# Kernel tuning notes

Hardware: AMD Instinct MI355X
Metric: run time of the kernel (lower is better)

The kernel has to match this reference:

```python
import jax, jax.numpy as jnp
import numpy as np

# dims
B, N, D = 2, 4096, 384
NUM_HEADS, KEY_DIM, VALUE_DIM = 8, 48, 48
TOP_K = 128
IDX_HEADS, IDX_DIM = 2, 32
SCALE = KEY_DIM ** (-0.5)


def setup_inputs() -> dict:
    key = jax.random.key(0)
    ks = jax.random.split(key, 9)
    def xavier(k, shape):
        fan_in, fan_out = shape[0], shape[1]
        lim = (6.0 / (fan_in + fan_out)) ** 0.5
        return jax.random.uniform(k, shape, jnp.float32, -lim, lim)
    return {
        "x": jax.random.normal(ks[0], (B, N, D), jnp.float32),
        # lightning indexer params
        "wq_idx": xavier(ks[1], (D, IDX_HEADS * IDX_DIM)),
        "wk_idx": xavier(ks[2], (D, IDX_DIM)),
        "ww_idx": xavier(ks[3], (D, IDX_HEADS)),
        # attention params (stored as (in, out) for x @ W)
        "wq": xavier(ks[4], (D, NUM_HEADS * KEY_DIM)),
        "wk": xavier(ks[5], (D, KEY_DIM)),
        "wv": xavier(ks[6], (D, VALUE_DIM)),
        "wo": xavier(ks[7], (NUM_HEADS * VALUE_DIM, D)),
    }


def _forward(x, wq_idx, wk_idx, ww_idx, wq, wk, wv, wo):
    b, n, d = x.shape
    # ---- Lightning indexer: I[q,s] = sum_h w[q,h] * relu(qi[q,h] . ki[s]) ----
    qi = (x @ wq_idx).reshape(b, n, IDX_HEADS, IDX_DIM)      # (B,N,Hi,dki)
    ki = x @ wk_idx                                           # (B,N,dki)
    w_idx = x @ ww_idx                                        # (B,N,Hi)
    raw = jax.nn.relu(jnp.einsum('bqhd,bsd->bqhs', qi, ki))   # (B,Nq,Hi,Nk)
    index_scores = jnp.einsum('bqhs,bqh->bqs', raw, w_idx)    # (B,Nq,Nk)

    # ---- MQA projections ----
    q = (x @ wq).reshape(b, n, NUM_HEADS, KEY_DIM).transpose(0, 2, 1, 3)  # (B,H,N,dk)
    k = x @ wk                                                # (B,N,dk) single KV head
    v = x @ wv                                                # (B,N,dv)

    # ---- top-k select + gather ----
    kk = min(TOP_K, n)
    _, top_idx = jax.lax.top_k(index_scores, kk)              # (B,Nq,k)
    bidx = jnp.arange(b)[:, None, None]
    sel_k = k[bidx, top_idx]                                  # (B,Nq,k,dk)
    sel_v = v[bidx, top_idx]                                  # (B,Nq,k,dv)

    # ---- sparse attention over selected keys ----
    attn = jnp.einsum('bhqd,bqkd->bhqk', q, sel_k) * SCALE    # (B,H,Nq,k)
    probs = jax.nn.softmax(attn, axis=-1)
    out = jnp.einsum('bhqk,bqkd->bhqd', probs, sel_v)         # (B,H,Nq,dv)
    out = out.transpose(0, 2, 1, 3).reshape(b, n, NUM_HEADS * VALUE_DIM)
    return out @ wo                                           # (B,N,D)


def reference(x, wq_idx, wk_idx, ww_idx, wq, wk, wv, wo):
    return _forward(x, wq_idx, wk_idx, ww_idx, wq, wk, wv, wo)
```

## Files before the change

### kernel.cpp

```cpp
#include <hip/hip_runtime.h>
#include <math.h>

#define NB 2
#define NSEQ 4096
#define DMODEL 384
#define NH 8
#define DKQ 48
#define DV 48
#define TOPK 128
#define NQ (NB*NSEQ)

#define QKV_COLS 480
#define C_Q 0
#define C_K 384
#define C_V 432
#define IDX_COLS 128
#define P_QI 0
#define P_KI 64
#define P_W  96
#define ATT_SCALE 0.14433756729740643f

typedef double v4d  __attribute__((ext_vector_type(4)));
typedef float  f32x4 __attribute__((ext_vector_type(4)));
typedef short  s16x8 __attribute__((ext_vector_type(8)));

__device__ inline void bsplit(float v, unsigned short& h, unsigned short& l) {
    unsigned hb = __float_as_uint(v);
    unsigned short hi = (unsigned short)((hb + 0x7FFFu + ((hb >> 16) & 1u)) >> 16);
    float hf = __uint_as_float(((unsigned)hi) << 16);
    float r = v - hf;
    unsigned rb = __float_as_uint(r);
    unsigned short lo = (unsigned short)((rb + 0x7FFFu + ((rb >> 16) & 1u)) >> 16);
    h = hi; l = lo;
}

__global__ void k_split(const float* __restrict__ x,
                        unsigned short* __restrict__ xhi, unsigned short* __restrict__ xlo) {
    int i = blockIdx.x * 256 + threadIdx.x;
    if (i < NQ * DMODEL) {
        unsigned short h, l;
        bsplit(x[i], h, l);
        xhi[i] = h; xlo[i] = l;
    }
}

__global__ void k_concat(const float* __restrict__ wq_idx, const float* __restrict__ wk_idx,
                         const float* __restrict__ ww_idx, const float* __restrict__ wq,
                         const float* __restrict__ wk, const float* __restrict__ wv,
                         const float* __restrict__ wo,
                         unsigned short* __restrict__ WqT_hi, unsigned short* __restrict__ WqT_lo,
                         unsigned short* __restrict__ WoT_hi, unsigned short* __restrict__ WoT_lo,
                         float* __restrict__ Wi_cat) {
    int i = blockIdx.x * 256 + threadIdx.x;
    const int NQK = QKV_COLS * DMODEL;
    const int NWO = DMODEL * DMODEL;
    if (i < NQK) {
        int n = i / DMODEL, k = i % DMODEL;
        float v;
        if (n < 384)      v = wq[(size_t)k*384 + n];
        else if (n < 432) v = wk[(size_t)k*48 + (n-384)];
        else              v = wv[(size_t)k*48 + (n-432)];
        unsigned short h, l; bsplit(v, h, l);
        WqT_hi[i] = h; WqT_lo[i] = l;
    } else if (i < NQK + NWO) {
        int j = i - NQK;
        int n = j / DMODEL, k = j % DMODEL;
        float v = wo[(size_t)k*384 + n];
        unsigned short h, l; bsplit(v, h, l);
        WoT_hi[j] = h; WoT_lo[j] = l;
    } else if (i < NQK + NWO + DMODEL*IDX_COLS) {
        int j = i - NQK - NWO;
        int d = j / IDX_COLS, c = j % IDX_COLS;
        float v;
        if (c < 64)       v = wq_idx[d*64 + c];
        else if (c < 96)  v = wk_idx[d*32 + (c-64)];
        else if (c < 98)  v = ww_idx[d*2 + (c-96)];
        else              v = 0.f;
        Wi_cat[j] = v;
    }
}

#define GLDK 40
__global__ __launch_bounds__(256) void k_gemm_mfma(
        const unsigned short* __restrict__ Ahi, const unsigned short* __restrict__ Alo,
        const unsigned short* __restrict__ Bhi, const unsigned short* __restrict__ Blo,
        float* __restrict__ C, int N, int ldc) {
    __shared__ unsigned short At[2][128][GLDK];
    __shared__ unsigned short Bt[2][64][GLDK];
    const int t = threadIdx.x;
    const int lane = t & 63, wid = t >> 6;
    const int row0 = blockIdx.y * 128, col0 = blockIdx.x * 64;
    const int ml = lane & 15, kq = lane >> 4;
    const int wm = (wid & 1) * 64, wn = (wid >> 1) * 32;

    unsigned short mv = (unsigned short)(__float_as_uint((float)(ml + 1)) >> 16);
    unsigned short one = 0x3F80;
    s16x8 pa, pb;
    #pragma unroll
    for (int j = 0; j < 8; j++) { pa[j] = (short)mv; pb[j] = (short)one; }
    f32x4 zf = (f32x4){0.f, 0.f, 0.f, 0.f};
    f32x4 rowp = __builtin_amdgcn_mfma_f32_16x16x32_bf16(pa, pb, zf, 0, 0, 0);
    f32x4 colp = __builtin_amdgcn_mfma_f32_16x16x32_bf16(pb, pa, zf, 0, 0, 0);
    int rowm[4], colm[4];
    #pragma unroll
    for (int r = 0; r < 4; r++) {
        rowm[r] = (((int)(rowp[r] * 0.03125f + 0.5f)) - 1) & 15;
        colm[r] = (((int)(colp[r] * 0.03125f + 0.5f)) - 1) & 15;
    }

    f32x4 acc[4][2];
    #pragma unroll
    for (int mt = 0; mt < 4; mt++)
        #pragma unroll
        for (int nt = 0; nt < 2; nt++) acc[mt][nt] = zf;

    for (int k0 = 0; k0 < DMODEL; k0 += 32) {
        #pragma unroll
        for (int i = 0; i < 4; i++) {
            int ch = t + 256*i;
            int arr = ch >> 9, rem = ch & 511;
            int r = rem >> 2, p = rem & 3;
            const unsigned short* src = arr ? Alo : Ahi;
            *(int4*)&At[arr][r][p*8] = *(const int4*)(src + (size_t)(row0 + r)*DMODEL + k0 + p*8);
        }
        #pragma unroll
        for (int i = 0; i < 2; i++) {
            int ch = t + 256*i;
            int arr = ch >> 8, rem = ch & 255;
            int r = rem >> 2, p = rem & 3;
            const unsigned short* src = arr ? Blo : Bhi;
            int gc = col0 + r;
            int4 v = {0, 0, 0, 0};
            if (gc < N) v = *(const int4*)(src + (size_t)gc*DMODEL + k0 + p*8);
            *(int4*)&Bt[arr][r][p*8] = v;
        }
        __syncthreads();
        s16x8 af[4][2], bfr[2][2];
        #pragma unroll
        for (int mt = 0; mt < 4; mt++)
            #pragma unroll
            for (int h = 0; h < 2; h++)
                af[mt][h] = *(const s16x8*)&At[h][wm + mt*16 + ml][kq*8];
        #pragma unroll
        for (int nt = 0; nt < 2; nt++)
            #pragma unroll
            for (int h = 0; h < 2; h++)
                bfr[nt][h] = *(const s16x8*)&Bt[h][wn + nt*16 + ml][kq*8];
        #pragma unroll
        for (int mt = 0; mt < 4; mt++)
            #pragma unroll
            for (int nt = 0; nt < 2; nt++) {
                acc[mt][nt] = __builtin_amdgcn_mfma_f32_16x16x32_bf16(af[mt][0], bfr[nt][0], acc[mt][nt], 0, 0, 0);
                acc[mt][nt] = __builtin_amdgcn_mfma_f32_16x16x32_bf16(af[mt][0], bfr[nt][1], acc[mt][nt], 0, 0, 0);
                acc[mt][nt] = __builtin_amdgcn_mfma_f32_16x16x32_bf16(af[mt][1], bfr[nt][0], acc[mt][nt], 0, 0, 0);
            }
        __syncthreads();
    }
    #pragma unroll
    for (int mt = 0; mt < 4; mt++)
        #pragma unroll
        for (int nt = 0; nt < 2; nt++)
            #pragma unroll
            for (int r = 0; r < 4; r++) {
                int rr = row0 + wm + mt*16 + rowm[r];
                int cc = col0 + wn + nt*16 + colm[r];
                if (cc < N) C[(size_t)rr*ldc + cc] = acc[mt][nt][r];
            }
}

__global__ __launch_bounds__(256) void k_proj64(const float* __restrict__ A,
                                                const float* __restrict__ W,
                                                double* __restrict__ P) {
    __shared__ float At[16][32];
    __shared__ float Bt[16][IDX_COLS];
    const int t  = threadIdx.x;
    const int tx = t & 15;
    const int ty = t >> 4;
    const int row0 = blockIdx.x * 32;
    double acc[2][8] = {};

    for (int k0 = 0; k0 < DMODEL; k0 += 16) {
        if (t < 128) {
            int m = t >> 2, kc = t & 3;
            float4 a = *(const float4*)(A + (size_t)(row0 + m)*DMODEL + k0 + kc*4);
            At[kc*4+0][m] = a.x; At[kc*4+1][m] = a.y;
            At[kc*4+2][m] = a.z; At[kc*4+3][m] = a.w;
        }
        for (int i = 0; i < 2; i++) {
            int lin = t + i*256;
            int kk = lin >> 5, c4 = lin & 31;
            float4 b = *(const float4*)(W + (size_t)(k0+kk)*IDX_COLS + c4*4);
            *(float4*)&Bt[kk][c4*4] = b;
        }
        __syncthreads();
        for (int kk = 0; kk < 16; kk++) {
            float a2[2], b8[8];
            a2[0] = At[kk][ty*2]; a2[1] = At[kk][ty*2+1];
            *(float4*)&b8[0] = *(const float4*)&Bt[kk][tx*8];
            *(float4*)&b8[4] = *(const float4*)&Bt[kk][tx*8+4];
            for (int i = 0; i < 2; i++)
                for (int j = 0; j < 8; j++)
                    acc[i][j] += (double)a2[i] * (double)b8[j];
        }
        __syncthreads();
    }
    for (int i = 0; i < 2; i++)
        for (int j = 0; j < 8; j++)
            P[(size_t)(row0 + ty*2 + i)*IDX_COLS + tx*8 + j] = acc[i][j];
}

__global__ __launch_bounds__(256) void k_score_mfma(const double* __restrict__ P,
                                                    unsigned int* __restrict__ K32,
                                                    unsigned int* __restrict__ L32,
                                                    int qstart) {
    __shared__ double A0[32][33];
    __shared__ double A1[32][33];
    __shared__ double Bk[32][129];
    __shared__ double wsh[2][32];
    const int t = threadIdx.x;
    const int lane = t & 63;
    const int wid = t >> 6;
    const int g0 = qstart + blockIdx.y * 32;
    const int b  = g0 / NSEQ;
    const int s0 = blockIdx.x * 128;

    for (int i = 0; i < 8; i++) {
        int lin = t + i*256;
        int q = lin >> 6, c = lin & 63;
        double v = P[(size_t)(g0 + q)*IDX_COLS + P_QI + c];
        if (c < 32) A0[c][q] = v; else A1[c-32][q] = v;
    }
    for (int i = 0; i < 16; i++) {
        int lin = t + i*256;
        int s = lin >> 5, c = lin & 31;
        Bk[c][s] = P[(size_t)(b*NSEQ + s0 + s)*IDX_COLS + P_KI + c];
    }
    if (t < 64) wsh[t & 1][t >> 1] = P[(size_t)(g0 + (t >> 1))*IDX_COLS + P_W + (t & 1)];

    const int qw = (wid & 1) * 16;
    const int sw = (wid >> 1) * 64;
    const int ml = lane & 15;
    const int kl = lane >> 4;

    v4d zero = (v4d){0.0, 0.0, 0.0, 0.0};
    v4d rowp = __builtin_amdgcn_mfma_f64_16x16x4f64((double)(ml+1), 1.0, zero, 0, 0, 0);
    v4d colp = __builtin_amdgcn_mfma_f64_16x16x4f64(1.0, (double)(ml+1), zero, 0, 0, 0);
    int rowm[4], colm[4];
    #pragma unroll
    for (int r = 0; r < 4; r++) {
        rowm[r] = (((int)(rowp[r] * 0.25 + 0.5)) - 1) & 15;
        colm[r] = (((int)(colp[r] * 0.25 + 0.5)) - 1) & 15;
    }

    __syncthreads();

    v4d acc0[4], acc1[4];
    #pragma unroll
    for (int st = 0; st < 4; st++) { acc0[st] = zero; acc1[st] = zero; }

    #pragma unroll
    for (int k4 = 0; k4 < 8; k4++) {
        int k = k4*4 + kl;
        double a0 = A0[k][qw + ml];
        double a1 = A1[k][qw + ml];
        #pragma unroll
        for (int st = 0; st < 4; st++) {
            double bb = Bk[k][sw + st*16 + ml];
            acc0[st] = __builtin_amdgcn_mfma_f64_16x16x4f64(a0, bb, acc0[st], 0, 0, 0);
            acc1[st] = __builtin_amdgcn_mfma_f64_16x16x4f64(a1, bb, acc1[st], 0, 0, 0);
        }
    }

    #pragma unroll
    for (int reg = 0; reg < 4; reg++) {
        int q = qw + rowm[reg];
        double w0 = wsh[0][q], w1 = wsh[1][q];
        #pragma unroll
        for (int st = 0; st < 4; st++) {
            double sc = w0 * fmax(acc0[st][reg], 0.0) + w1 * fmax(acc1[st][reg], 0.0);
            size_t oidx = (size_t)(blockIdx.y*32 + q)*NSEQ + s0 + sw + st*16 + colm[reg];
            unsigned long long bb = (unsigned long long)__double_as_longlong(sc);
            unsigned long long u = (bb & 0x8000000000000000ULL) ? ~bb : (bb | 0x8000000000000000ULL);
            K32[oidx] = (unsigned int)(u >> 32);
            L32[oidx] = (unsigned int)u;
        }
    }
}

__global__ __launch_bounds__(256) void k_topk(const unsigned int* __restrict__ K32,
                                              const unsigned int* __restrict__ L32,
                                              int* __restrict__ IDX, int qstart) {
    __shared__ unsigned int hist[4][256];
    __shared__ unsigned int wred[4];
    __shared__ unsigned int s_b, s_need, s_flag, s_cnt;
    const int t = threadIdx.x, lane = t & 63;
    const int wid = t >> 6;
    const int q = blockIdx.x;
    const unsigned int* krow = K32 + (size_t)q * NSEQ;
    const unsigned int* lrow = L32 + (size_t)q * NSEQ;
    int* orow = IDX + (size_t)(qstart + q) * TOPK;

    unsigned int kr[16];
    #pragma unroll
    for (int jj = 0; jj < 4; jj++) {
        uint4 v = *(const uint4*)(krow + (t*4 + 1024*jj));
        kr[jj*4+0] = v.x; kr[jj*4+1] = v.y; kr[jj*4+2] = v.z; kr[jj*4+3] = v.w;
    }

    unsigned int mymax = kr[0];
    #pragma unroll
    for (int j = 1; j < 16; j++) mymax = kr[j] > mymax ? kr[j] : mymax;

    if (t == 0) { s_cnt = 0; s_need = TOPK; }

    auto clearhist = [&]() {
        #pragma unroll
        for (int w = 0; w < 4; w++) hist[w][t] = 0;
        __syncthreads();
    };
    auto decide = [&]() {
        if (wid == 0) {
            unsigned int c[4];
            #pragma unroll
            for (int k2 = 0; k2 < 4; k2++)
                c[k2] = hist[0][lane*4+k2] + hist[1][lane*4+k2]
                      + hist[2][lane*4+k2] + hist[3][lane*4+k2];
            unsigned int run = c[0] + c[1] + c[2] + c[3];
            #pragma unroll
            for (int d2 = 1; d2 < 64; d2 <<= 1) {
                unsigned int v = __shfl_down(run, d2, 64);
                if (lane + d2 < 64) run += v;
            }
            unsigned int need = s_need;
            unsigned int Sb[5];
            Sb[0] = run; Sb[1] = run - c[0]; Sb[2] = Sb[1] - c[1];
            Sb[3] = Sb[2] - c[2]; Sb[4] = Sb[3] - c[3];
            #pragma unroll
            for (int j = 0; j < 4; j++) {
                if (Sb[j] >= need && Sb[j+1] < need) {
                    s_b = (unsigned int)(lane*4 + j);
                    s_need = need - Sb[j+1];
                    s_flag = (need - Sb[j+1] == c[j]) ? 1u : 0u;
                }
            }
        }
        __syncthreads();
    };

    clearhist();
    atomicAdd(&hist[wid][mymax >> 24], 1u);
    __syncthreads();
    decide();
    const unsigned int B1 = s_b;

    clearhist();
    if ((mymax >> 24) == B1) atomicAdd(&hist[wid][(mymax >> 16) & 255u], 1u);
    __syncthreads();
    decide();
    const unsigned int T16 = (B1 << 8) | s_b;

    unsigned int amask = 0;
    #pragma unroll
    for (int j = 0; j < 16; j++)
        if ((kr[j] >> 16) >= T16) amask |= (1u << j);

    if (t == 0) s_need = TOPK;

    #pragma unroll 1
    for (int stage = 0; stage < 2; ++stage) {
        #pragma unroll 1
        for (int level = 0; level < 4; ++level) {
            const int sh = 24 - 8*level;
            clearhist();

            #pragma unroll
            for (int j = 0; j < 16; j++) {
                if ((amask >> j) & 1u)
                    atomicAdd(&hist[wid][(kr[j] >> sh) & 255u], 1u);
            }
            __syncthreads();
            decide();
            const unsigned int bstar = s_b;

            if (s_flag) {
                #pragma unroll
                for (int j = 0; j < 16; j++) {
                    if (((amask >> j) & 1u) && (((kr[j] >> sh) & 255u) >= bstar))
                        orow[atomicAdd(&s_cnt, 1u)] = (j >> 2)*1024 + t*4 + (j & 3);
                }
                return;
            }
            unsigned int nm = 0;
            #pragma unroll
            for (int j = 0; j < 16; j++) {
                if ((amask >> j) & 1u) {
                    unsigned int d = (kr[j] >> sh) & 255u;
                    if (d > bstar) orow[atomicAdd(&s_cnt, 1u)] = (j >> 2)*1024 + t*4 + (j & 3);
                    else if (d == bstar) nm |= (1u << j);
                }
            }
            amask = nm;
        }
        if (stage == 0) {
            #pragma unroll
            for (int jj = 0; jj < 4; jj++) {
                if ((amask >> (jj*4)) & 0xFu) {
                    uint4 v = *(const uint4*)(lrow + (t*4 + 1024*jj));
                    kr[jj*4+0] = v.x; kr[jj*4+1] = v.y; kr[jj*4+2] = v.z; kr[jj*4+3] = v.w;
                }
            }
        }
    }

    const unsigned int needF = s_need;
    unsigned int base = 0;
    #pragma unroll 1
    for (int jj = 0; jj < 4; jj++) {
        unsigned int m4 = (amask >> (jj*4)) & 0xFu;
        unsigned int cnt = __popc(m4);
        unsigned int inc = cnt;
        #pragma unroll
        for (int d2 = 1; d2 < 64; d2 <<= 1) {
            unsigned int v = __shfl_up(inc, d2, 64);
            if (lane >= d2) inc += v;
        }
        if (lane == 63) wred[wid] = inc;
        __syncthreads();
        unsigned int woff = 0;
        for (int w2 = 0; w2 < wid; w2++) woff += wred[w2];
        unsigned int T = wred[0] + wred[1] + wred[2] + wred[3];
        unsigned int p = base + woff + inc - cnt;
        #pragma unroll
        for (int c = 0; c < 4; c++) {
            if ((m4 >> c) & 1u) {
                if (p < needF) orow[atomicAdd(&s_cnt, 1u)] = jj*1024 + t*4 + c;
                p++;
            }
        }
        base += T;
        __syncthreads();
    }
}

#define KVP 52
__global__ __launch_bounds__(256) void k_attn_qk(const float* __restrict__ Y,
                                                 const int* __restrict__ IDX,
                                                 float* __restrict__ Pr) {
    __shared__ float Ks[TOPK][KVP];
    __shared__ float qsh[NH*DKQ];
    __shared__ int   idxs[TOPK];
    const int g = blockIdx.x;
    const int b = g / NSEQ;
    const int t = threadIdx.x;

    if (t < TOPK) idxs[t] = IDX[(size_t)g*TOPK + t];
    for (int i = t; i < NH*DKQ; i += 256) qsh[i] = Y[(size_t)g*QKV_COLS + C_Q + i];
    __syncthreads();
    #pragma unroll
    for (int i = 0; i < 6; i++) {
        int e = t + 256*i;
        int j = e / 12, p = e % 12;
        const float* src = Y + (size_t)(b*NSEQ + idxs[j])*QKV_COLS + C_K;
        *(float4*)&Ks[j][p*4] = *(const float4*)(src + p*4);
    }
    __syncthreads();

    const int h  = t >> 5;
    const int j0 = t & 31;
    float lo[4] = {0.f, 0.f, 0.f, 0.f};
    #pragma unroll
    for (int c = 0; c < 12; c++) {
        float4 qv = *(const float4*)&qsh[h*DKQ + c*4];
        #pragma unroll
        for (int i = 0; i < 4; i++) {
            float4 kv = *(const float4*)&Ks[j0 + 32*i][c*4];
            lo[i] += qv.x*kv.x + qv.y*kv.y + qv.z*kv.z + qv.w*kv.w;
        }
    }
    #pragma unroll
    for (int i = 0; i < 4; i++) lo[i] *= ATT_SCALE;
    float m = fmaxf(fmaxf(lo[0], lo[1]), fmaxf(lo[2], lo[3]));
    for (int d = 16; d >= 1; d >>= 1) m = fmaxf(m, __shfl_xor(m, d, 64));
    float e0[4], sum = 0.f;
    #pragma unroll
    for (int i = 0; i < 4; i++) { e0[i] = __expf(lo[i] - m); sum += e0[i]; }
    for (int d = 16; d >= 1; d >>= 1) sum += __shfl_xor(sum, d, 64);
    float inv = 1.0f / sum;
    #pragma unroll
    for (int i = 0; i < 4; i++)
        Pr[(size_t)g*(NH*TOPK) + h*TOPK + j0 + 32*i] = e0[i] * inv;
}

__global__ __launch_bounds__(256) void k_attn_pv(const float* __restrict__ Y,
                                                 const int* __restrict__ IDX,
                                                 const float* __restrict__ Pr,
                                                 unsigned short* __restrict__ ctx_hi,
                                                 unsigned short* __restrict__ ctx_lo) {
    __shared__ float Vs[TOPK][KVP];
    __shared__ float prs[NH*TOPK];
    __shared__ int   idxs[TOPK];
    const int g = blockIdx.x;
    const int b = g / NSEQ;
    const int t = threadIdx.x;

    if (t < TOPK) idxs[t] = IDX[(size_t)g*TOPK + t];
    *(float4*)&prs[t*4] = *(const float4*)(Pr + (size_t)g*(NH*TOPK) + t*4);
    __syncthreads();
    #pragma unroll
    for (int i = 0; i < 6; i++) {
        int e = t + 256*i;
        int j = e / 12, p = e % 12;
        const float* src = Y + (size_t)(b*NSEQ + idxs[j])*QKV_COLS + C_V;
        *(float4*)&Vs[j][p*4] = *(const float4*)(src + p*4);
    }
    __syncthreads();

    for (int o = t; o < NH*DV; o += 256) {
        int hh = o / DV, dd = o % DV;
        float acc = 0.f;
        #pragma unroll
        for (int jc = 0; jc < 32; jc++) {
            float4 pv = *(const float4*)&prs[hh*TOPK + jc*4];
            acc += pv.x*Vs[jc*4+0][dd] + pv.y*Vs[jc*4+1][dd]
                 + pv.z*Vs[jc*4+2][dd] + pv.w*Vs[jc*4+3][dd];
        }
        unsigned short h, l;
        bsplit(acc, h, l);
        ctx_hi[(size_t)g*(NH*DV) + o] = h;
        ctx_lo[(size_t)g*(NH*DV) + o] = l;
    }
}

extern "C" void kernel_launch(void* const* d_in, const int* in_sizes, int n_in,
                              void* d_out, int out_size, void* d_ws, size_t ws_size,
                              hipStream_t stream) {
    const float* x      = (const float*)d_in[0];
    const float* wq_idx = (const float*)d_in[1];
    const float* wk_idx = (const float*)d_in[2];
    const float* ww_idx = (const float*)d_in[3];
    const float* wq     = (const float*)d_in[4];
    const float* wk     = (const float*)d_in[5];
    const float* wv     = (const float*)d_in[6];
    const float* wo     = (const float*)d_in[7];
    float* out = (float*)d_out;
    char*  ws  = (char*)d_ws;

    size_t off = 0;
    auto carve = [&](size_t bytes) { size_t o = off; off = (off + bytes + 255) & ~(size_t)255; return o; };
    size_t oWqh = carve((size_t)QKV_COLS*DMODEL*2);
    size_t oWql = carve((size_t)QKV_COLS*DMODEL*2);
    size_t oWoh = carve((size_t)DMODEL*DMODEL*2);
    size_t oWol = carve((size_t)DMODEL*DMODEL*2);
    size_t oWi  = carve((size_t)DMODEL*IDX_COLS*4);
    size_t oXh  = carve((size_t)NQ*DMODEL*2);
    size_t oXl  = carve((size_t)NQ*DMODEL*2);
    size_t oY   = carve((size_t)NQ*QKV_COLS*4);
    size_t oP   = carve((size_t)NQ*IDX_COLS*8);
    size_t oIdx = carve((size_t)NQ*TOPK*4);
    size_t oPr  = carve((size_t)NQ*NH*TOPK*4);
    size_t oCh  = carve((size_t)NQ*NH*DV*2);
    size_t oCl  = carve((size_t)NQ*NH*DV*2);
    size_t oKL  = off;

    int QC = NSEQ;
    while (QC > 32 && oKL + (size_t)QC*NSEQ*8 > ws_size) QC >>= 1;

    unsigned short* WqT_hi = (unsigned short*)(ws + oWqh);
    unsigned short* WqT_lo = (unsigned short*)(ws + oWql);
    unsigned short* WoT_hi = (unsigned short*)(ws + oWoh);
    unsigned short* WoT_lo = (unsigned short*)(ws + oWol);
    float*  Wi_cat = (float*)(ws + oWi);
    unsigned short* xhi = (unsigned short*)(ws + oXh);
    unsigned short* xlo = (unsigned short*)(ws + oXl);
    float*  Y      = (float*)(ws + oY);
    double* P      = (double*)(ws + oP);
    int*    IDX    = (int*)(ws + oIdx);
    float*  Pr     = (float*)(ws + oPr);
    unsigned short* ctx_hi = (unsigned short*)(ws + oCh);
    unsigned short* ctx_lo = (unsigned short*)(ws + oCl);
    unsigned int* K32 = (unsigned int*)(ws + oKL);
    unsigned int* L32 = (unsigned int*)(ws + oKL + (size_t)QC*NSEQ*4);

    int ncat = QKV_COLS*DMODEL + DMODEL*DMODEL + DMODEL*IDX_COLS;
    k_split<<<(NQ*DMODEL + 255)/256, 256, 0, stream>>>(x, xhi, xlo);
    k_concat<<<(ncat + 255)/256, 256, 0, stream>>>(wq_idx, wk_idx, ww_idx, wq, wk, wv, wo,
                                                   WqT_hi, WqT_lo, WoT_hi, WoT_lo, Wi_cat);
    k_gemm_mfma<<<dim3((QKV_COLS + 63)/64, NQ/128), 256, 0, stream>>>(xhi, xlo, WqT_hi, WqT_lo, Y, QKV_COLS, QKV_COLS);
    k_proj64<<<NQ/32, 256, 0, stream>>>(x, Wi_cat, P);
    for (int qs = 0; qs < NQ; qs += QC) {
        k_score_mfma<<<dim3(NSEQ/128, QC/32), 256, 0, stream>>>(P, K32, L32, qs);
        k_topk<<<QC, 256, 0, stream>>>(K32, L32, IDX, qs);
    }
    k_attn_qk<<<NQ, 256, 0, stream>>>(Y, IDX, Pr);
    k_attn_pv<<<NQ, 256, 0, stream>>>(Y, IDX, Pr, ctx_hi, ctx_lo);
    k_gemm_mfma<<<dim3(DMODEL/64, NQ/128), 256, 0, stream>>>(ctx_hi, ctx_lo, WoT_hi, WoT_lo, out, DMODEL, DMODEL);
}
```

Before: 542.6 us.

## Replace histogram radix top-k with ballot-based candidate compaction and bitwise threshold search

Computes the prefilter threshold with per-wave ballot bit-search over per-thread maxima instead of two shared histogram passes, then compacts candidates into shared memory. When at most 512 candidates survive, a single wave finds the exact 128th key by a 32-bit ballot binary search, breaking ties with the low word and then the index, and writes the outputs. This avoids repeated histogram clears, atomics and block barriers per radix level. The fallback keeps the old histogram path, and only one wave is busy during the fast path.

```diff
diff --git a/kernel.cpp b/kernel.cpp
--- a/kernel.cpp
+++ b/kernel.cpp
@@ -292,7 +292,9 @@
                                               int* __restrict__ IDX, int qstart) {
     __shared__ unsigned int hist[4][256];
     __shared__ unsigned int wred[4];
-    __shared__ unsigned int s_b, s_need, s_flag, s_cnt;
+    __shared__ unsigned int s_b, s_need, s_flag, s_cnt, s_n;
+    __shared__ unsigned int CK[512];
+    __shared__ int CI[512];
     const int t = threadIdx.x, lane = t & 63;
     const int wid = t >> 6;
     const int q = blockIdx.x;
@@ -306,12 +308,133 @@
         uint4 v = *(const uint4*)(krow + (t*4 + 1024*jj));
         kr[jj*4+0] = v.x; kr[jj*4+1] = v.y; kr[jj*4+2] = v.z; kr[jj*4+3] = v.w;
     }
-
     unsigned int mymax = kr[0];
     #pragma unroll
     for (int j = 1; j < 16; j++) mymax = kr[j] > mymax ? kr[j] : mymax;
-
-    if (t == 0) { s_cnt = 0; s_need = TOPK; }
+    const unsigned int p16 = mymax >> 16;
+
+    unsigned int Tw = 0;
+    #pragma unroll
+    for (int bit = 15; bit >= 0; --bit) {
+        unsigned int trial = Tw | (1u << bit);
+        if (__popcll(__ballot(p16 >= trial)) >= 32) Tw = trial;
+    }
+    if (lane == 0) wred[wid] = Tw;
+    if (t == 0) { s_cnt = 0; s_n = 0; s_need = TOPK; s_flag = 0; }
+    __syncthreads();
+    unsigned int T16 = wred[0];
+    T16 = wred[1] < T16 ? wred[1] : T16;
+    T16 = wred[2] < T16 ? wred[2] : T16;
+    T16 = wred[3] < T16 ? wred[3] : T16;
+
+    #pragma unroll
+    for (int j = 0; j < 16; j++) {
+        if ((kr[j] >> 16) >= T16) {
+            unsigned int pos = atomicAdd(&s_n, 1u);
+            if (pos < 512u) { CK[pos] = kr[j]; CI[pos] = (j >> 2)*1024 + t*4 + (j & 3); }
+        }
+    }
+    __syncthreads();
+    const unsigned int n = s_n;
+
+    if (n <= 512u) {
+        if (wid == 0) {
+            unsigned int ck[8]; bool cv[8];
+            #pragma unroll
+            for (int e = 0; e < 8; e++) {
+                int id = lane + e*64;
+                cv[e] = (unsigned int)id < n;
+                ck[e] = cv[e] ? CK[id] : 0u;
+            }
+            unsigned int T = 0;
+            for (int bit = 31; bit >= 0; --bit) {
+                unsigned int trial = T | (1u << bit);
+                unsigned int c = 0;
+                #pragma unroll
+                for (int e = 0; e < 8; e++)
+                    c += (unsigned int)__popcll(__ballot(cv[e] && ck[e] >= trial));
+                if (c >= (unsigned int)TOPK) T = trial;
+            }
+            unsigned int G = 0, E = 0;
+            #pragma unroll
+            for (int e = 0; e < 8; e++) {
+                G += (unsigned int)__popcll(__ballot(cv[e] && ck[e] > T));
+                E += (unsigned int)__popcll(__ballot(cv[e] && ck[e] == T));
+            }
+            const unsigned int need = (unsigned int)TOPK - G;
+            const unsigned long long ltm = (1ull << lane) - 1ull;
+
+            unsigned int cbase = 0;
+            #pragma unroll
+            for (int e = 0; e < 8; e++) {
+                bool em = cv[e] && ck[e] > T;
+                unsigned long long m = __ballot(em);
+                if (em) orow[cbase + __popcll(m & ltm)] = CI[lane + e*64];
+                cbase += (unsigned int)__popcll(m);
+            }
+            if (E == need) {
+                #pragma unroll
+                for (int e = 0; e < 8; e++) {
+                    bool em = cv[e] && ck[e] == T;
+                    unsigned long long m = __ballot(em);
+                    if (em) orow[cbase + __popcll(m & ltm)] = CI[lane + e*64];
+                    cbase += (unsigned int)__popcll(m);
+                }
+            } else {
+                unsigned int lo[8]; bool tv[8];
+                #pragma unroll
+                for (int e = 0; e < 8; e++) {
+                    tv[e] = cv[e] && ck[e] == T;
+                    lo[e] = tv[e] ? lrow[CI[lane + e*64]] : 0u;
+                }
+                unsigned int L = 0;
+                for (int bit = 31; bit >= 0; --bit) {
+                    unsigned int trial = L | (1u << bit);
+                    unsigned int c = 0;
+                    #pragma unroll
+                    for (int e = 0; e < 8; e++)
+                        c += (unsigned int)__popcll(__ballot(tv[e] && lo[e] >= trial));
+                    if (c >= need) L = trial;
+                }
+                unsigned int G2 = 0;
+                #pragma unroll
+                for (int e = 0; e < 8; e++)
+                    G2 += (unsigned int)__popcll(__ballot(tv[e] && lo[e] > L));
+                #pragma unroll
+                for (int e = 0; e < 8; e++) {
+                    bool em = tv[e] && lo[e] > L;
+                    unsigned long long m = __ballot(em);
+                    if (em) orow[cbase + __popcll(m & ltm)] = CI[lane + e*64];
+                    cbase += (unsigned int)__popcll(m);
+                }
+                const unsigned int need3 = need - G2;
+                unsigned int r = 0;
+                for (int bit = 11; bit >= 0; --bit) {
+                    unsigned int trial = r | (1u << bit);
+                    unsigned int c = 0;
+                    #pragma unroll
+                    for (int e = 0; e < 8; e++)
+                        c += (unsigned int)__popcll(__ballot(tv[e] && lo[e] == L &&
+                                 (unsigned int)CI[lane + e*64] <= trial));
+                    if (c <= need3) r = trial;
+                }
+                #pragma unroll
+                for (int e = 0; e < 8; e++) {
+                    int idv = CI[lane + e*64];
+                    bool em = tv[e] && lo[e] == L && (unsigned int)idv <= r;
+                    unsigned long long m = __ballot(em);
+                    if (em) orow[cbase + __popcll(m & ltm)] = idv;
+                    cbase += (unsigned int)__popcll(m);
+                }
+            }
+        }
+        return;
+    }
+
+    unsigned int amask = 0;
+    #pragma unroll
+    for (int j = 0; j < 16; j++)
+        if ((kr[j] >> 16) >= T16) amask |= (1u << j);
 
     auto clearhist = [&]() {
         #pragma unroll
@@ -347,32 +470,12 @@
         __syncthreads();
     };
 
-    clearhist();
-    atomicAdd(&hist[wid][mymax >> 24], 1u);
-    __syncthreads();
-    decide();
-    const unsigned int B1 = s_b;
-
-    clearhist();
-    if ((mymax >> 24) == B1) atomicAdd(&hist[wid][(mymax >> 16) & 255u], 1u);
-    __syncthreads();
-    decide();
-    const unsigned int T16 = (B1 << 8) | s_b;
-
-    unsigned int amask = 0;
-    #pragma unroll
-    for (int j = 0; j < 16; j++)
-        if ((kr[j] >> 16) >= T16) amask |= (1u << j);
-
-    if (t == 0) s_need = TOPK;
-
     #pragma unroll 1
     for (int stage = 0; stage < 2; ++stage) {
         #pragma unroll 1
         for (int level = 0; level < 4; ++level) {
             const int sh = 24 - 8*level;
             clearhist();
-
             #pragma unroll
             for (int j = 0; j < 16; j++) {
                 if ((amask >> j) & 1u)
```

After: 537.0 us. About the same (-1.0%).
